# Optimization experiments

Hardware: AMD Instinct MI355X
Metric: run time of the kernel (lower is better)

The kernel has to match this reference:

```python
import jax, jax.numpy as jnp
import numpy as np

B, S, HID = 2, 2048, 2304
H, KVH, D = 8, 4, 256          # query heads, kv heads, head_dim
N_REP = H // KVH
SCALE = 256.0 ** -0.5          # query_pre_attn_scalar ** -0.5
SOFTCAP = 50.0
ROPE_THETA = 10000.0
NEG = -1e9


def setup_inputs() -> dict:
    key = jax.random.key(0)
    k1, k2, k3, k4, k5 = jax.random.split(key, 5)
    hidden_states = jax.random.normal(k1, (B, S, HID), dtype=jnp.float32)
    # RoPE cos/sin tables, shape [B, S, D]
    inv_freq = 1.0 / (ROPE_THETA ** (jnp.arange(0, D, 2, dtype=jnp.float32) / D))
    pos = jnp.arange(S, dtype=jnp.float32)
    freqs = pos[:, None] * inv_freq[None, :]            # [S, D/2]
    emb = jnp.concatenate([freqs, freqs], axis=-1)      # [S, D]
    cos = jnp.broadcast_to(jnp.cos(emb)[None], (B, S, D))
    sin = jnp.broadcast_to(jnp.sin(emb)[None], (B, S, D))
    # additive causal mask [B, 1, S, S] (sliding_window=4096 > S, so pure causal)
    idx = jnp.arange(S)
    causal = idx[None, :] <= idx[:, None]
    attention_mask = jnp.broadcast_to(
        jnp.where(causal, 0.0, NEG).astype(jnp.float32)[None, None], (B, 1, S, S))
    # projection weights (lecun-normal-ish scale), no bias (attention_bias=False)
    Wq = jax.random.normal(k2, (HID, H * D), dtype=jnp.float32) / np.sqrt(HID)
    Wk = jax.random.normal(k3, (HID, KVH * D), dtype=jnp.float32) / np.sqrt(HID)
    Wv = jax.random.normal(k4, (HID, KVH * D), dtype=jnp.float32) / np.sqrt(HID)
    Wo = jax.random.normal(k5, (H * D, HID), dtype=jnp.float32) / np.sqrt(H * D)
    return {"hidden_states": hidden_states, "cos": cos, "sin": sin,
            "attention_mask": attention_mask,
            "Wq": Wq, "Wk": Wk, "Wv": Wv, "Wo": Wo}


def _rotate_half(x):
    half = x.shape[-1] // 2
    return jnp.concatenate([-x[..., half:], x[..., :half]], axis=-1)


def reference(hidden_states, cos, sin, attention_mask, Wq, Wk, Wv, Wo):
    b, s, _ = hidden_states.shape
    q = (hidden_states @ Wq).reshape(b, s, H, D).transpose(0, 2, 1, 3)    # [B,H,S,D]
    k = (hidden_states @ Wk).reshape(b, s, KVH, D).transpose(0, 2, 1, 3)  # [B,KVH,S,D]
    v = (hidden_states @ Wv).reshape(b, s, KVH, D).transpose(0, 2, 1, 3)
    c = cos[:, None]  # [B,1,S,D] broadcast over heads (unsqueeze_dim=1)
    sn = sin[:, None]
    q = q * c + _rotate_half(q) * sn
    k = k * c + _rotate_half(k) * sn
    # GQA: repeat kv heads (interleave, matching repeat_kv tile+reshape)
    k = jnp.repeat(k, N_REP, axis=1)
    v = jnp.repeat(v, N_REP, axis=1)
    w = jnp.einsum('bhqd,bhkd->bhqk', q, k) * SCALE
    w = jnp.tanh(w / SOFTCAP) * SOFTCAP                  # logit softcapping
    w = w + attention_mask[:, :, :, :s]
    w = jax.nn.softmax(w.astype(jnp.float32), axis=-1).astype(q.dtype)
    out = jnp.einsum('bhqk,bhkd->bhqd', w, v)
    out = out.transpose(0, 2, 1, 3).reshape(b, s, H * D)
    return out @ Wo
```

## Files before the change

kernel.cpp:

```cpp
#include <hip/hip_runtime.h>

typedef unsigned short u16;
typedef __attribute__((ext_vector_type(8))) short short8;
typedef __attribute__((ext_vector_type(4))) float f32x4;

constexpr int B_ = 2;
constexpr int H_ = 8;
constexpr int KVH_ = 4;
constexpr int S_ = 2048;
constexpr int D_ = 256;
constexpr int HID_ = 2304;
constexpr int QKVN_ = 4096;
constexpr int AON_ = 2048;

__device__ __forceinline__ float b2f(u16 u) {
  union { float f; unsigned int i; } x; x.i = ((unsigned int)u) << 16; return x.f;
}
__device__ __forceinline__ u16 f2b(float f) {
  unsigned int x = __float_as_uint(f);
  unsigned int r = (x + 0x7fffu + ((x >> 16) & 1u)) >> 16;
  return (u16)r;
}

__global__ void cast_kernel(const float* __restrict__ in, u16* __restrict__ out) {
  size_t i = ((size_t)blockIdx.x * 256 + threadIdx.x) * 4;
  float4 v = *(const float4*)(in + i);
  unsigned int lo = (unsigned int)f2b(v.x) | ((unsigned int)f2b(v.y) << 16);
  unsigned int hi = (unsigned int)f2b(v.z) | ((unsigned int)f2b(v.w) << 16);
  uint2 o; o.x = lo; o.y = hi;
  *(uint2*)(out + i) = o;
}

__global__ void transpose_cast_all(const float* __restrict__ s0, const float* __restrict__ s1,
                                   const float* __restrict__ s2, const float* __restrict__ s3,
                                   u16* __restrict__ d0, u16* __restrict__ d1,
                                   u16* __restrict__ d2, u16* __restrict__ d3) {
  __shared__ float tile[64][65];
  int which = blockIdx.z;
  const float* src; u16* dst; int R, C;
  if (which == 0)      { src = s0; dst = d0; R = 2304; C = 2048; }
  else if (which == 1) { src = s1; dst = d1; R = 2304; C = 1024; }
  else if (which == 2) { src = s2; dst = d2; R = 2304; C = 1024; }
  else                 { src = s3; dst = d3; R = 2048; C = 2304; }
  int r0 = blockIdx.y * 64, c0 = blockIdx.x * 64;
  if (r0 >= R || c0 >= C) return;
  int t = threadIdx.x;
#pragma unroll
  for (int i = 0; i < 16; ++i) {
    int e = i * 256 + t;
    int r = e >> 6, c = e & 63;
    tile[r][c] = src[(size_t)(r0 + r) * C + (c0 + c)];
  }
  __syncthreads();
#pragma unroll
  for (int i = 0; i < 16; ++i) {
    int e = i * 256 + t;
    int orow = e >> 6, ocol = e & 63;
    dst[(size_t)(c0 + orow) * R + (r0 + ocol)] = f2b(tile[ocol][orow]);
  }
}

template <int OUTF32>
__global__ __launch_bounds__(512, 2) void gemm_bt8(
    const u16* __restrict__ A, const u16* __restrict__ B, void* __restrict__ Cp,
    int M, int N, int K) {
  __shared__ u16 lds[2][2][2][8192];
  const int tid = threadIdx.x;
  const int lane = tid & 63;
  const int wave = tid >> 6;
  const int wm = wave >> 2, wn = wave & 3;
  const int quad = lane >> 4, l16 = lane & 15;
  const int m0 = blockIdx.y * 256, n0 = blockIdx.x * 256;
  const int nt = K >> 6;

  const int sub = tid >> 6;
  const int rr = (tid >> 2) & 15;
  const int cc = ((tid & 3) * 8) ^ ((rr & 8) ? 16 : 0);
  const int r_rel = (sub >> 1) * 16 + rr;
  const int ccol = (sub & 1) * 32 + cc;
  const u16* Asrc = A + (size_t)(m0 + r_rel) * K + ccol;
  const u16* Bsrc = B + (size_t)(n0 + r_rel) * K + ccol;
  const int ldsc = tid * 8;

  const int fr_off = l16 * 64 + (((quad * 8) ^ ((l16 & 8) ? 16 : 0)) << 1);

#define GL8(src, dst)                                                                  \
  __builtin_amdgcn_global_load_lds((const __attribute__((address_space(1))) void*)(src), \
                                   (__attribute__((address_space(3))) void*)(dst), 16, 0, 0)
#define STAGE_A(bf, kt, qp) {                                                          \
    const u16* _s = Asrc + (size_t)(kt) * 64;                                          \
    GL8(_s + (size_t)((qp) * 64) * K,       &lds[bf][0][0][(qp) * 4096 + ldsc]);       \
    GL8(_s + (size_t)(128 + (qp) * 64) * K, &lds[bf][0][1][(qp) * 4096 + ldsc]); }
#define STAGE_B(bf, kt, hf) {                                                          \
    const u16* _s = Bsrc + (size_t)(kt) * 64;                                          \
    GL8(_s + (size_t)((hf) * 128) * K,      &lds[bf][1][hf][ldsc]);                    \
    GL8(_s + (size_t)((hf) * 128 + 64) * K, &lds[bf][1][hf][4096 + ldsc]); }
#define LDA(bf, mi, kk) \
  (*(const short8*)((const char*)&lds[bf][0][wm][0] + (mi) * 2048 + (kk) * 1024 + fr_off))
#define LDB(bf, ni, kk) \
  (*(const short8*)((const char*)&lds[bf][1][wn >> 1][0] + ((wn & 1) * 4 + (ni)) * 2048 + (kk) * 1024 + fr_off))

  f32x4 acc[8][4] = {};
  short8 bfr[4][2], af[2][2];

  STAGE_B(0, 0, 0); STAGE_B(0, 0, 1); STAGE_A(0, 0, 0); STAGE_A(0, 0, 1);
  STAGE_B(1, 1, 0); STAGE_B(1, 1, 1); STAGE_A(1, 1, 0);
  asm volatile("s_waitcnt vmcnt(6)" ::: "memory");
  __builtin_amdgcn_s_barrier();

#define PHASE(q, STG, VMW)                                                             \
    _Pragma("unroll") for (int i = 0; i < 2; ++i)                                      \
      _Pragma("unroll") for (int kk = 0; kk < 2; ++kk) af[i][kk] = LDA(c, 2 * (q) + i, kk); \
    STG; VMW;                                                                          \
    __builtin_amdgcn_s_barrier();                                                      \
    asm volatile("s_waitcnt lgkmcnt(0)" ::: "memory");                                 \
    __builtin_amdgcn_sched_barrier(0);                                                 \
    __builtin_amdgcn_s_setprio(1);                                                     \
    _Pragma("unroll") for (int i = 0; i < 2; ++i)                                      \
      _Pragma("unroll") for (int ni = 0; ni < 4; ++ni)                                 \
        _Pragma("unroll") for (int kk = 0; kk < 2; ++kk)                               \
          acc[2 * (q) + i][ni] = __builtin_amdgcn_mfma_f32_16x16x32_bf16(              \
              af[i][kk], bfr[ni][kk], acc[2 * (q) + i][ni], 0, 0, 0);                  \
    __builtin_amdgcn_s_setprio(0);                                                     \
    __builtin_amdgcn_s_barrier();

  for (int T = 0; T < nt; ++T) {
    const int c = T & 1;
#pragma unroll
    for (int ni = 0; ni < 4; ++ni)
#pragma unroll
      for (int kk = 0; kk < 2; ++kk) bfr[ni][kk] = LDB(c, ni, kk);
    PHASE(0, if (T + 1 < nt) STAGE_A(c ^ 1, T + 1, 1), )
    PHASE(1, if (T + 2 < nt) STAGE_B(c, T + 2, 0), )
    PHASE(2, if (T + 2 < nt) STAGE_B(c, T + 2, 1), )
    PHASE(3, if (T + 2 < nt) STAGE_A(c, T + 2, 0),
          if (T + 2 >= nt) { asm volatile("s_waitcnt vmcnt(0)" ::: "memory"); }
          else             { asm volatile("s_waitcnt vmcnt(6)" ::: "memory"); })
  }
#undef PHASE
#undef LDA
#undef LDB
#undef STAGE_A
#undef STAGE_B
#undef GL8

#pragma unroll
  for (int mi = 0; mi < 8; ++mi) {
#pragma unroll
    for (int ni = 0; ni < 4; ++ni) {
#pragma unroll
      for (int r = 0; r < 4; ++r) {
        int row = m0 + wm * 128 + mi * 16 + quad * 4 + r;
        int col = n0 + wn * 64 + ni * 16 + l16;
        if (OUTF32)
          ((float*)Cp)[(size_t)row * N + col] = acc[mi][ni][r];
        else
          ((u16*)Cp)[(size_t)row * N + col] = f2b(acc[mi][ni][r]);
      }
    }
  }
}

__global__ void rope_kernel(const u16* __restrict__ qkv, const float* __restrict__ cs,
                            const float* __restrict__ sn, u16* __restrict__ Qr,
                            u16* __restrict__ Kr) {
  int row = blockIdx.x;
  int b = row >> 11, s = row & 2047;
  int d = threadIdx.x;
  const u16* qrow = qkv + (size_t)row * QKVN_;
  float c = cs[(size_t)row * D_ + d];
  float si = sn[(size_t)row * D_ + d];
  int dp = (d < 128) ? d + 128 : d - 128;
  float sgn = (d < 128) ? -1.f : 1.f;
#pragma unroll
  for (int h = 0; h < H_; ++h) {
    float v = b2f(qrow[h * D_ + d]);
    float p = sgn * b2f(qrow[h * D_ + dp]);
    Qr[((size_t)(b * H_ + h) * S_ + s) * D_ + d] = f2b(v * c + p * si);
  }
#pragma unroll
  for (int g = 0; g < KVH_; ++g) {
    float v = b2f(qrow[2048 + g * D_ + d]);
    float p = sgn * b2f(qrow[2048 + g * D_ + dp]);
    Kr[((size_t)(b * KVH_ + g) * S_ + s) * D_ + d] = f2b(v * c + p * si);
  }
}

__global__ void transpose_v(const u16* __restrict__ qkv, u16* __restrict__ Vt) {
  __shared__ u16 tile[64][72];
  int d0 = blockIdx.x * 64, s0 = blockIdx.y * 64, g = blockIdx.z;
  int b = g >> 2, kvh = g & 3;
  int t = threadIdx.x;
#pragma unroll
  for (int i = 0; i < 16; ++i) {
    int e = i * 256 + t;
    int r = e >> 6, c = e & 63;
    tile[r][c] = qkv[(size_t)(b * S_ + s0 + r) * QKVN_ + 3072 + kvh * D_ + d0 + c];
  }
  __syncthreads();
#pragma unroll
  for (int i = 0; i < 16; ++i) {
    int e = i * 256 + t;
    int orow = e >> 6, ocol = e & 63;
    Vt[((size_t)g * D_ + d0 + orow) * S_ + s0 + ocol] = tile[ocol][orow];
  }
}

__global__ __launch_bounds__(256, 2) void attn_kernel(
    const u16* __restrict__ Qr, const u16* __restrict__ Kr, const u16* __restrict__ Vt,
    float* __restrict__ Op0, float* __restrict__ Op1,
    float* __restrict__ Lp0, float* __restrict__ Lp1) {
  __shared__ u16 Ks[2][32 * 256];
  __shared__ u16 Vs[2][32 * 256];
  int u = blockIdx.x >> 1, sp = blockIdx.x & 1;
  int h = blockIdx.y;
  int kvh = h >> 1;
  int tid = threadIdx.x, wave = tid >> 6, lane = tid & 63;
  int quad = lane >> 4, l16 = lane & 15;
  float* Op = sp ? Op1 : Op0;
  float* Lp = sp ? Lp1 : Lp0;
  int ksrc_s[4], ksrc_c[4], vsrc_d[4], vsrc_s[4];
#pragma unroll
  for (int i = 0; i < 4; ++i) {
    int p = i * 256 + tid;
    int sK = p >> 5;
    ksrc_s[i] = sK;
    ksrc_c[i] = (p & 31) ^ ((sK & 3) | (((sK >> 3) & 1) << 2));
    vsrc_d[i] = p >> 2;
    vsrc_s[i] = (p & 3) ^ ((p >> 3) & 3);
  }
  const int kg = l16 >> 2, ka = l16 & 3;
  const int srow0 = 8 * kg + ka;
  const int ksw = ka | ((kg & 1) << 2);

  for (int part = 0; part < 2; ++part) {
    int b = part;
    int qt = (part == 0) ? u : (31 - u);
    int q0 = qt * 64;
    int beg = sp ? (qt + 1) : 0;
    int end = sp ? (2 * qt + 2) : (qt + 1);
    const u16* Qbase = Qr + ((size_t)(b * H_ + h) * S_ + q0 + wave * 16 + l16) * D_;
    short8 qf[8];
#pragma unroll
    for (int kk = 0; kk < 8; ++kk)
      qf[kk] = *(const short8*)(Qbase + kk * 32 + quad * 8);
    const u16* Kbase = Kr + (size_t)(b * KVH_ + kvh) * S_ * D_;
    const u16* Vbase = Vt + (size_t)(b * KVH_ + kvh) * D_ * S_;
    float lp = 0.f;
    f32x4 o_acc[16] = {};
    const int qq = q0 + wave * 16 + l16;

#define STAGE(KT, BUF)                                                                   \
    {                                                                                    \
      int k0s = (KT) * 32;                                                               \
      _Pragma("unroll") for (int i = 0; i < 4; ++i) {                                    \
        int p = i * 256 + tid;                                                           \
        __builtin_amdgcn_global_load_lds(                                                \
            (const __attribute__((address_space(1))) void*)(Kbase +                      \
                (size_t)(k0s + ksrc_s[i]) * D_ + ksrc_c[i] * 8),                         \
            (__attribute__((address_space(3))) void*)(&Ks[BUF][0] + p * 8), 16, 0, 0);   \
      }                                                                                  \
      _Pragma("unroll") for (int i = 0; i < 4; ++i) {                                    \
        int p = i * 256 + tid;                                                           \
        __builtin_amdgcn_global_load_lds(                                                \
            (const __attribute__((address_space(1))) void*)(Vbase +                      \
                (size_t)vsrc_d[i] * S_ + k0s + vsrc_s[i] * 8),                           \
            (__attribute__((address_space(3))) void*)(&Vs[BUF][0] + p * 8), 16, 0, 0);   \
      }                                                                                  \
    }

    STAGE(beg, 0);
    __syncthreads();
    for (int kt = beg; kt < end; ++kt) {
      int k0 = kt * 32;
      int cur = (kt - beg) & 1;
      if (kt + 1 < end) STAGE(kt + 1, cur ^ 1);
      f32x4 sacc[2] = {};
      __builtin_amdgcn_s_setprio(1);
#pragma unroll
      for (int n = 0; n < 2; ++n) {
        const u16* kb = &Ks[cur][0] + (srow0 + 4 * n) * 256;
#pragma unroll
        for (int kk = 0; kk < 8; ++kk) {
          int phys = (kk * 4 + quad) ^ ksw;
          short8 kfr = *(const short8*)(kb + phys * 8);
          sacc[n] = __builtin_amdgcn_mfma_f32_16x16x32_bf16(kfr, qf[kk], sacc[n], 0, 0, 0);
        }
      }
      __builtin_amdgcn_s_setprio(0);
      bool full = (k0 + 31 <= q0 + wave * 16);
#pragma unroll
      for (int n = 0; n < 2; ++n) {
#pragma unroll
        for (int r = 0; r < 4; ++r) {
          float E = __expf(sacc[n][r] * 0.0025f);
          float ee = __expf(-100.0f * __frcp_rn(E + 1.0f));
          if (!full) {
            int key = k0 + 8 * quad + 4 * n + r;
            ee = (key <= qq) ? ee : 0.0f;
          }
          lp += ee;
          sacc[n][r] = ee;
        }
      }
      union { short8 s8; unsigned int d[4]; } pu;
      pu.d[0] = (unsigned int)f2b(sacc[0][0]) | ((unsigned int)f2b(sacc[0][1]) << 16);
      pu.d[1] = (unsigned int)f2b(sacc[0][2]) | ((unsigned int)f2b(sacc[0][3]) << 16);
      pu.d[2] = (unsigned int)f2b(sacc[1][0]) | ((unsigned int)f2b(sacc[1][1]) << 16);
      pu.d[3] = (unsigned int)f2b(sacc[1][2]) | ((unsigned int)f2b(sacc[1][3]) << 16);
      short8 pa = pu.s8;
      __builtin_amdgcn_s_setprio(1);
#pragma unroll
      for (int dt = 0; dt < 16; ++dt) {
        int d = dt * 16 + l16;
        int phys = quad ^ ((d >> 1) & 3);
        short8 vb = *(const short8*)(&Vs[cur][0] + d * 32 + phys * 8);
        o_acc[dt] = __builtin_amdgcn_mfma_f32_16x16x32_bf16(pa, vb, o_acc[dt], 0, 0, 0);
      }
      __builtin_amdgcn_s_setprio(0);
      __syncthreads();
    }
#undef STAGE
    lp += __shfl_xor(lp, 16, 64);
    lp += __shfl_xor(lp, 32, 64);
    if (lane < 16)
      Lp[((size_t)(b * H_ + h)) * S_ + q0 + wave * 16 + lane] = lp;
#pragma unroll
    for (int dt = 0; dt < 16; ++dt)
#pragma unroll
      for (int r = 0; r < 4; ++r) {
        int row = b * S_ + q0 + wave * 16 + quad * 4 + r;
        int col = h * D_ + dt * 16 + l16;
        Op[(size_t)row * AON_ + col] = o_acc[dt][r];
      }
  }
}

__global__ void combine_kernel(const float* __restrict__ Op0, const float* __restrict__ Op1,
                               const float* __restrict__ Lp0, const float* __restrict__ Lp1,
                               u16* __restrict__ Ao) {
  size_t idx = (size_t)blockIdx.x * 256 + threadIdx.x;
  size_t row = idx >> 9;
  int c4 = ((int)idx & 511) * 4;
  const float4 a = *(const float4*)(Op0 + row * AON_ + c4);
  const float4 b4 = *(const float4*)(Op1 + row * AON_ + c4);
  int b = (int)(row >> 11), s = (int)row & 2047;
  int h = c4 >> 8;
  size_t li = ((size_t)(b * H_ + h)) * S_ + s;
  float inv = 1.0f / (Lp0[li] + Lp1[li]);
  unsigned int lo = (unsigned int)f2b((a.x + b4.x) * inv) | ((unsigned int)f2b((a.y + b4.y) * inv) << 16);
  unsigned int hi = (unsigned int)f2b((a.z + b4.z) * inv) | ((unsigned int)f2b((a.w + b4.w) * inv) << 16);
  uint2 o; o.x = lo; o.y = hi;
  *(uint2*)(Ao + row * AON_ + c4) = o;
}

extern "C" void kernel_launch(void* const* d_in, const int* in_sizes, int n_in,
                              void* d_out, int out_size, void* d_ws, size_t ws_size,
                              hipStream_t stream) {
  const float* hidden = (const float*)d_in[0];
  const float* cosp = (const float*)d_in[1];
  const float* sinp = (const float*)d_in[2];
  const float* Wq = (const float*)d_in[4];
  const float* Wk = (const float*)d_in[5];
  const float* Wv = (const float*)d_in[6];
  const float* Wo = (const float*)d_in[7];

  u16* hs  = (u16*)d_ws;
  u16* WT  = hs  + (size_t)4096 * HID_;
  u16* WoT = WT  + (size_t)4096 * HID_;
  u16* qkv = WoT + (size_t)HID_ * AON_;
  u16* Qr  = qkv + (size_t)4096 * QKVN_;
  u16* Kr  = Qr  + (size_t)B_ * H_ * S_ * D_;
  u16* Vt  = Kr  + (size_t)B_ * KVH_ * S_ * D_;
  u16* Ao  = Vt  + (size_t)B_ * KVH_ * S_ * D_;
  float* Lp0 = (float*)(Ao + (size_t)4096 * AON_);
  float* Lp1 = Lp0 + (size_t)B_ * H_ * S_;
  float* Op0 = (float*)hs;
  float* Op1 = (float*)qkv;

  cast_kernel<<<9216, 256, 0, stream>>>(hidden, hs);
  transpose_cast_all<<<dim3(36, 36, 4), 256, 0, stream>>>(
      Wq, Wk, Wv, Wo, WT, WT + (size_t)2048 * HID_, WT + (size_t)3072 * HID_, WoT);
  gemm_bt8<0><<<dim3(16, 16), 512, 0, stream>>>(hs, WT, qkv, 4096, QKVN_, HID_);
  rope_kernel<<<4096, 256, 0, stream>>>(qkv, cosp, sinp, Qr, Kr);
  transpose_v<<<dim3(4, 32, 8), 256, 0, stream>>>(qkv, Vt);
  attn_kernel<<<dim3(64, 8), 256, 0, stream>>>(Qr, Kr, Vt, Op0, Op1, Lp0, Lp1);
  combine_kernel<<<16384, 256, 0, stream>>>(Op0, Op1, Lp0, Lp1, Ao);
  gemm_bt8<1><<<dim3(9, 16), 512, 0, stream>>>(Ao, WoT, d_out, 4096, HID_, 2048);
}
```

Measured before the change: 405.4 us.

## Double query rows per wave in attention to reuse K/V tiles

Each wave now processes 32 query rows (two 16-row fragments) instead of 16, so every K and V fragment read from LDS feeds two MFMAs. The query tile grows to 128 rows and the grid halves to 32x8 blocks. Launch bounds drop to one block per SM to make room for the doubled accumulator registers, and the staging address math is simplified to per-thread constants. Fewer blocks (256 on a large-CU GPU) and lower occupancy may reduce latency hiding and leave compute units underused.

```diff
diff --git a/kernel.cpp b/kernel.cpp
--- a/kernel.cpp
+++ b/kernel.cpp
@@ -206,7 +206,7 @@
   }
 }
 
-__global__ __launch_bounds__(256, 2) void attn_kernel(
+__global__ __launch_bounds__(256, 1) void attn_kernel(
     const u16* __restrict__ Qr, const u16* __restrict__ Kr, const u16* __restrict__ Vt,
     float* __restrict__ Op0, float* __restrict__ Op1,
     float* __restrict__ Lp0, float* __restrict__ Lp1) {
@@ -219,36 +219,32 @@
   int quad = lane >> 4, l16 = lane & 15;
   float* Op = sp ? Op1 : Op0;
   float* Lp = sp ? Lp1 : Lp0;
-  int ksrc_s[4], ksrc_c[4], vsrc_d[4], vsrc_s[4];
-#pragma unroll
-  for (int i = 0; i < 4; ++i) {
-    int p = i * 256 + tid;
-    int sK = p >> 5;
-    ksrc_s[i] = sK;
-    ksrc_c[i] = (p & 31) ^ ((sK & 3) | (((sK >> 3) & 1) << 2));
-    vsrc_d[i] = p >> 2;
-    vsrc_s[i] = (p & 3) ^ ((p >> 3) & 3);
-  }
+  const int kst_r = tid >> 5;
+  const int kst_c = (tid & 31) ^ ((tid >> 5) & 3);
+  const int vst_r = tid >> 2;
+  const int vst_c = (tid & 3) ^ ((tid >> 3) & 3);
   const int kg = l16 >> 2, ka = l16 & 3;
   const int srow0 = 8 * kg + ka;
   const int ksw = ka | ((kg & 1) << 2);
 
   for (int part = 0; part < 2; ++part) {
     int b = part;
-    int qt = (part == 0) ? u : (31 - u);
-    int q0 = qt * 64;
-    int beg = sp ? (qt + 1) : 0;
-    int end = sp ? (2 * qt + 2) : (qt + 1);
-    const u16* Qbase = Qr + ((size_t)(b * H_ + h) * S_ + q0 + wave * 16 + l16) * D_;
-    short8 qf[8];
-#pragma unroll
-    for (int kk = 0; kk < 8; ++kk)
-      qf[kk] = *(const short8*)(Qbase + kk * 32 + quad * 8);
+    int qt = (part == 0) ? u : (15 - u);
+    int q0 = qt * 128;
+    int beg = sp ? (2 * qt + 2) : 0;
+    int end = sp ? (4 * qt + 4) : (2 * qt + 2);
+    const u16* Qbase = Qr + ((size_t)(b * H_ + h) * S_ + q0 + wave * 32 + l16) * D_;
+    short8 qf[2][8];
+#pragma unroll
+    for (int f = 0; f < 2; ++f)
+#pragma unroll
+      for (int kk = 0; kk < 8; ++kk)
+        qf[f][kk] = *(const short8*)(Qbase + (size_t)f * 16 * D_ + kk * 32 + quad * 8);
     const u16* Kbase = Kr + (size_t)(b * KVH_ + kvh) * S_ * D_;
     const u16* Vbase = Vt + (size_t)(b * KVH_ + kvh) * D_ * S_;
-    float lp = 0.f;
-    f32x4 o_acc[16] = {};
-    const int qq = q0 + wave * 16 + l16;
+    float lp[2] = {0.f, 0.f};
+    f32x4 o_acc[2][16] = {};
+    const int qq0 = q0 + wave * 32 + l16;
 
 #define STAGE(KT, BUF)                                                                   \
     {                                                                                    \
@@ -257,14 +253,14 @@
         int p = i * 256 + tid;                                                           \
         __builtin_amdgcn_global_load_lds(                                                \
             (const __attribute__((address_space(1))) void*)(Kbase +                      \
-                (size_t)(k0s + ksrc_s[i]) * D_ + ksrc_c[i] * 8),                         \
+                (size_t)(k0s + i * 8 + kst_r) * D_ + (kst_c ^ ((i & 1) << 2)) * 8),      \
             (__attribute__((address_space(3))) void*)(&Ks[BUF][0] + p * 8), 16, 0, 0);   \
       }                                                                                  \
       _Pragma("unroll") for (int i = 0; i < 4; ++i) {                                    \
         int p = i * 256 + tid;                                                           \
         __builtin_amdgcn_global_load_lds(                                                \
             (const __attribute__((address_space(1))) void*)(Vbase +                      \
-                (size_t)vsrc_d[i] * S_ + k0s + vsrc_s[i] * 8),                           \
+                (size_t)(i * 64 + vst_r) * S_ + k0s + vst_c * 8),                        \
             (__attribute__((address_space(3))) void*)(&Vs[BUF][0] + p * 8), 16, 0, 0);   \
       }                                                                                  \
     }
@@ -275,7 +271,7 @@
       int k0 = kt * 32;
       int cur = (kt - beg) & 1;
       if (kt + 1 < end) STAGE(kt + 1, cur ^ 1);
-      f32x4 sacc[2] = {};
+      f32x4 sacc[2][2] = {};
       __builtin_amdgcn_s_setprio(1);
 #pragma unroll
       for (int n = 0; n < 2; ++n) {
@@ -284,55 +280,67 @@
         for (int kk = 0; kk < 8; ++kk) {
           int phys = (kk * 4 + quad) ^ ksw;
           short8 kfr = *(const short8*)(kb + phys * 8);
-          sacc[n] = __builtin_amdgcn_mfma_f32_16x16x32_bf16(kfr, qf[kk], sacc[n], 0, 0, 0);
+          sacc[0][n] = __builtin_amdgcn_mfma_f32_16x16x32_bf16(kfr, qf[0][kk], sacc[0][n], 0, 0, 0);
+          sacc[1][n] = __builtin_amdgcn_mfma_f32_16x16x32_bf16(kfr, qf[1][kk], sacc[1][n], 0, 0, 0);
         }
       }
       __builtin_amdgcn_s_setprio(0);
-      bool full = (k0 + 31 <= q0 + wave * 16);
-#pragma unroll
-      for (int n = 0; n < 2; ++n) {
-#pragma unroll
-        for (int r = 0; r < 4; ++r) {
-          float E = __expf(sacc[n][r] * 0.0025f);
-          float ee = __expf(-100.0f * __frcp_rn(E + 1.0f));
-          if (!full) {
-            int key = k0 + 8 * quad + 4 * n + r;
-            ee = (key <= qq) ? ee : 0.0f;
+      bool full = (k0 + 31 <= q0 + wave * 32);
+      short8 pa[2];
+#pragma unroll
+      for (int f = 0; f < 2; ++f) {
+        union { short8 s8; unsigned int d[4]; } pu;
+#pragma unroll
+        for (int n = 0; n < 2; ++n) {
+#pragma unroll
+          for (int r = 0; r < 4; ++r) {
+            float E = __expf(sacc[f][n][r] * 0.0025f);
+            float ee = __expf(-100.0f * __frcp_rn(E + 1.0f));
+            if (!full) {
+              int key = k0 + 8 * quad + 4 * n + r;
+              ee = (key <= qq0 + f * 16) ? ee : 0.0f;
+            }
+            lp[f] += ee;
+            sacc[f][n][r] = ee;
           }
-          lp += ee;
-          sacc[n][r] = ee;
+          pu.d[2 * n]     = (unsigned int)f2b(sacc[f][n][0]) | ((unsigned int)f2b(sacc[f][n][1]) << 16);
+          pu.d[2 * n + 1] = (unsigned int)f2b(sacc[f][n][2]) | ((unsigned int)f2b(sacc[f][n][3]) << 16);
         }
+        pa[f] = pu.s8;
       }
-      union { short8 s8; unsigned int d[4]; } pu;
-      pu.d[0] = (unsigned int)f2b(sacc[0][0]) | ((unsigned int)f2b(sacc[0][1]) << 16);
-      pu.d[1] = (unsigned int)f2b(sacc[0][2]) | ((unsigned int)f2b(sacc[0][3]) << 16);
-      pu.d[2] = (unsigned int)f2b(sacc[1][0]) | ((unsigned int)f2b(sacc[1][1]) << 16);
-      pu.d[3] = (unsigned int)f2b(sacc[1][2]) | ((unsigned int)f2b(sacc[1][3]) << 16);
-      short8 pa = pu.s8;
       __builtin_amdgcn_s_setprio(1);
 #pragma unroll
       for (int dt = 0; dt < 16; ++dt) {
         int d = dt * 16 + l16;
         int phys = quad ^ ((d >> 1) & 3);
         short8 vb = *(const short8*)(&Vs[cur][0] + d * 32 + phys * 8);
-        o_acc[dt] = __builtin_amdgcn_mfma_f32_16x16x32_bf16(pa, vb, o_acc[dt], 0, 0, 0);
+        o_acc[0][dt] = __builtin_amdgcn_mfma_f32_16x16x32_bf16(pa[0], vb, o_acc[0][dt], 0, 0, 0);
+        o_acc[1][dt] = __builtin_amdgcn_mfma_f32_16x16x32_bf16(pa[1], vb, o_acc[1][dt], 0, 0, 0);
       }
       __builtin_amdgcn_s_setprio(0);
       __syncthreads();
     }
 #undef STAGE
-    lp += __shfl_xor(lp, 16, 64);
-    lp += __shfl_xor(lp, 32, 64);
-    if (lane < 16)
-      Lp[((size_t)(b * H_ + h)) * S_ + q0 + wave * 16 + lane] = lp;
-#pragma unroll
-    for (int dt = 0; dt < 16; ++dt)
-#pragma unroll
-      for (int r = 0; r < 4; ++r) {
-        int row = b * S_ + q0 + wave * 16 + quad * 4 + r;
-        int col = h * D_ + dt * 16 + l16;
-        Op[(size_t)row * AON_ + col] = o_acc[dt][r];
-      }
+#pragma unroll
+    for (int f = 0; f < 2; ++f) {
+      lp[f] += __shfl_xor(lp[f], 16, 64);
+      lp[f] += __shfl_xor(lp[f], 32, 64);
+    }
+    if (lane < 16) {
+      size_t lb = ((size_t)(b * H_ + h)) * S_ + q0 + wave * 32 + lane;
+      Lp[lb] = lp[0];
+      Lp[lb + 16] = lp[1];
+    }
+#pragma unroll
+    for (int f = 0; f < 2; ++f)
+#pragma unroll
+      for (int dt = 0; dt < 16; ++dt)
+#pragma unroll
+        for (int r = 0; r < 4; ++r) {
+          int row = b * S_ + q0 + wave * 32 + f * 16 + quad * 4 + r;
+          int col = h * D_ + dt * 16 + l16;
+          Op[(size_t)row * AON_ + col] = o_acc[f][dt][r];
+        }
   }
 }
 
@@ -384,7 +392,7 @@
   gemm_bt8<0><<<dim3(16, 16), 512, 0, stream>>>(hs, WT, qkv, 4096, QKVN_, HID_);
   rope_kernel<<<4096, 256, 0, stream>>>(qkv, cosp, sinp, Qr, Kr);
   transpose_v<<<dim3(4, 32, 8), 256, 0, stream>>>(qkv, Vt);
-  attn_kernel<<<dim3(64, 8), 256, 0, stream>>>(Qr, Kr, Vt, Op0, Op1, Lp0, Lp1);
+  attn_kernel<<<dim3(32, 8), 256, 0, stream>>>(Qr, Kr, Vt, Op0, Op1, Lp0, Lp1);
   combine_kernel<<<16384, 256, 0, stream>>>(Op0, Op1, Lp0, Lp1, Ao);
   gemm_bt8<1><<<dim3(9, 16), 512, 0, stream>>>(Ao, WoT, d_out, 4096, HID_, 2048);
 }
```

Result: slower. 433.4 us (+6.9%).
